# Kernel tuning notes

Hardware: AMD Instinct MI355X
Metric: run time of the kernel (lower is better)

## Reference

```python
import jax, jax.numpy as jnp
import numpy as np

D = 768
OUT = 196
EPS = 1e-6


def setup_inputs() -> dict:
    key = jax.random.key(0)
    k_x, k_w, k_b, k_g, k_beta = jax.random.split(key, 5)
    x = jax.random.normal(k_x, (16, 4096, D), dtype=jnp.float32)
    # LayerNorm affine params
    gamma = jnp.ones((D,), dtype=jnp.float32) + 0.01 * jax.random.normal(k_g, (D,), dtype=jnp.float32)
    beta = 0.01 * jax.random.normal(k_beta, (D,), dtype=jnp.float32)
    # Linear params (torch default init: U(-1/sqrt(D), 1/sqrt(D)))
    bound = 1.0 / np.sqrt(D)
    W = jax.random.uniform(k_w, (OUT, D), minval=-bound, maxval=bound, dtype=jnp.float32)
    b = jax.random.uniform(k_b, (OUT,), minval=-bound, maxval=bound, dtype=jnp.float32)
    return {"x": x, "gamma": gamma, "beta": beta, "W": W, "b": b}


def reference(x, gamma, beta, W, b):
    # LayerNorm over last dim (768), eps=1e-6, elementwise affine
    mean = jnp.mean(x, axis=-1, keepdims=True)
    var = jnp.mean(jnp.square(x - mean), axis=-1, keepdims=True)
    xn = (x - mean) * jax.lax.rsqrt(var + EPS) * gamma + beta
    # Linear 768 -> 196
    return jnp.einsum('bsd,od->bso', xn, W) + b
```

## Files before the change

### kernel.cpp

```cpp
#include <hip/hip_runtime.h>

#define DD   768
#define OUTN 196
#define MT   16
#define APAD 776
#define KT   24

typedef __attribute__((ext_vector_type(8))) _Float16 halfx8;
typedef __attribute__((ext_vector_type(4))) _Float16 halfx4;
typedef __attribute__((ext_vector_type(4))) float    f32x4;

__global__ __launch_bounds__(256) void wprep_kernel(const float* __restrict__ W,
                                                    _Float16* __restrict__ Wh) {
    int i = blockIdx.x * 256 + threadIdx.x;
    if (i < OUTN * DD) Wh[i] = (_Float16)W[i];
}

__global__ __launch_bounds__(256) void fused_ln_linear(
    const float* __restrict__ x, const float* __restrict__ gamma,
    const float* __restrict__ beta, const _Float16* __restrict__ Wh,
    const float* __restrict__ bias, float* __restrict__ out)
{
    __shared__ _Float16 Ahi[MT * APAD];
    __shared__ _Float16 Alo[MT * APAD];

    const int tid  = threadIdx.x;
    const int wv   = tid >> 6;
    const int lane = tid & 63;
    const long row0 = (long)blockIdx.x * MT;

    float4 g[3], be[3];
#pragma unroll
    for (int c = 0; c < 3; ++c) {
        const int d0 = c * 256 + lane * 4;
        g[c]  = *(const float4*)(gamma + d0);
        be[c] = *(const float4*)(beta  + d0);
    }

    {
        float4 xv[4][3];
#pragma unroll
        for (int t = 0; t < 4; ++t) {
            const float* xp = x + (row0 + wv * 4 + t) * DD;
#pragma unroll
            for (int c = 0; c < 3; ++c)
                xv[t][c] = *(const float4*)(xp + c * 256 + lane * 4);
        }
#pragma unroll
        for (int t = 0; t < 4; ++t) {
            float s = 0.f, ss = 0.f;
#pragma unroll
            for (int c = 0; c < 3; ++c) {
                const float4 v = xv[t][c];
                s  += v.x + v.y + v.z + v.w;
                ss += v.x * v.x + v.y * v.y + v.z * v.z + v.w * v.w;
            }
#pragma unroll
            for (int off = 32; off > 0; off >>= 1) {
                s  += __shfl_xor(s,  off);
                ss += __shfl_xor(ss, off);
            }
            const float mean = s * (1.f / DD);
            const float var  = ss * (1.f / DD) - mean * mean;
            const float rstd = rsqrtf(var + 1e-6f);
            const int r = wv * 4 + t;
#pragma unroll
            for (int c = 0; c < 3; ++c) {
                const float4 v = xv[t][c];
                float y0 = (v.x - mean) * rstd * g[c].x + be[c].x;
                float y1 = (v.y - mean) * rstd * g[c].y + be[c].y;
                float y2 = (v.z - mean) * rstd * g[c].z + be[c].z;
                float y3 = (v.w - mean) * rstd * g[c].w + be[c].w;
                halfx4 hi, lo;
                hi[0] = (_Float16)y0; lo[0] = (_Float16)(y0 - (float)hi[0]);
                hi[1] = (_Float16)y1; lo[1] = (_Float16)(y1 - (float)hi[1]);
                hi[2] = (_Float16)y2; lo[2] = (_Float16)(y2 - (float)hi[2]);
                hi[3] = (_Float16)y3; lo[3] = (_Float16)(y3 - (float)hi[3]);
                const int k0 = c * 256 + lane * 4;
                *(halfx4*)(&Ahi[r * APAD + k0]) = hi;
                *(halfx4*)(&Alo[r * APAD + k0]) = lo;
            }
        }
    }
    __syncthreads();

    const int cnt  = (wv == 0) ? 4 : 3;
    const int nt0  = (wv == 0) ? 0 : (1 + 3 * wv);
    const int ln16 = lane & 15;
    const int q    = lane >> 4;

    f32x4 acc[4];
#pragma unroll
    for (int i = 0; i < 4; ++i) acc[i] = (f32x4){0.f, 0.f, 0.f, 0.f};

    int ncol[4], nload[4];
    float bs[4];
#pragma unroll
    for (int i = 0; i < 4; ++i) {
        const int n = (nt0 + i) * 16 + ln16;
        ncol[i]  = n;
        nload[i] = n < OUTN ? n : OUTN - 1;
        bs[i]    = (n < OUTN) ? bias[n] : 0.f;
    }

    const _Float16* Aph = &Ahi[ln16 * APAD + q * 8];
    const _Float16* Apl = &Alo[ln16 * APAD + q * 8];
#pragma unroll
    for (int kt = 0; kt < KT; ++kt) {
        const halfx8 ah = *(const halfx8*)(Aph + kt * 32);
        const halfx8 al = *(const halfx8*)(Apl + kt * 32);
#pragma unroll
        for (int i = 0; i < 4; ++i) {
            if (i < cnt) {
                const halfx8 bf = *(const halfx8*)(Wh + nload[i] * DD + kt * 32 + q * 8);
                acc[i] = __builtin_amdgcn_mfma_f32_16x16x32_f16(ah, bf, acc[i], 0, 0, 0);
                acc[i] = __builtin_amdgcn_mfma_f32_16x16x32_f16(al, bf, acc[i], 0, 0, 0);
            }
        }
    }

    const long rbase = row0 + q * 4;
#pragma unroll
    for (int i = 0; i < 4; ++i) {
        if (i < cnt && ncol[i] < OUTN) {
#pragma unroll
            for (int rg = 0; rg < 4; ++rg)
                out[(rbase + rg) * OUTN + ncol[i]] = acc[i][rg] + bs[i];
        }
    }
}

extern "C" void kernel_launch(void* const* d_in, const int* in_sizes, int n_in,
                              void* d_out, int out_size, void* d_ws, size_t ws_size,
                              hipStream_t stream) {
    const float* x     = (const float*)d_in[0];
    const float* gamma = (const float*)d_in[1];
    const float* beta  = (const float*)d_in[2];
    const float* W     = (const float*)d_in[3];
    const float* b     = (const float*)d_in[4];
    float* out = (float*)d_out;
    _Float16* Wh = (_Float16*)d_ws;

    wprep_kernel<<<(OUTN * DD + 255) / 256, 256, 0, stream>>>(W, Wh);

    const long rows = 16L * 4096;
    fused_ln_linear<<<rows / MT, 256, 0, stream>>>(x, gamma, beta, Wh, b, out);
}
```

Baseline: 433.7 us.

## Pipeline LayerNorm staging with GEMM over K chunks using double-buffered LDS

The fused kernel now makes two passes over x. The first pass computes the row statistics. The second pass normalizes one 256-wide K chunk at a time into double-buffered shared memory, and the MFMA work on the previous chunk overlaps the next chunk's normalization. This shrinks LDS per block and register pressure (launch bounds now request 4 blocks), so occupancy should rise, but x is read from global memory twice and relies on cache hits. The weight conversion kernel is also vectorized to float4.

After: 416.1 us. 4.1% less time.

```diff
diff --git a/kernel.cpp b/kernel.cpp
--- a/kernel.cpp
+++ b/kernel.cpp
@@ -1,97 +1,73 @@
 #include <hip/hip_runtime.h>
 
-#define DD   768
-#define OUTN 196
-#define MT   16
-#define APAD 776
-#define KT   24
+#define DD    768
+#define OUTN  196
+#define MT    16
+#define KC    256
+#define APAD  264
+#define KTS   8
 
 typedef __attribute__((ext_vector_type(8))) _Float16 halfx8;
 typedef __attribute__((ext_vector_type(4))) _Float16 halfx4;
 typedef __attribute__((ext_vector_type(4))) float    f32x4;
 
-__global__ __launch_bounds__(256) void wprep_kernel(const float* __restrict__ W,
-                                                    _Float16* __restrict__ Wh) {
+__global__ __launch_bounds__(256) void wprep_kernel(const float4* __restrict__ W4,
+                                                    halfx4* __restrict__ Wh4) {
     int i = blockIdx.x * 256 + threadIdx.x;
-    if (i < OUTN * DD) Wh[i] = (_Float16)W[i];
+    if (i < OUTN * DD / 4) {
+        float4 v = W4[i];
+        halfx4 h;
+        h[0] = (_Float16)v.x; h[1] = (_Float16)v.y;
+        h[2] = (_Float16)v.z; h[3] = (_Float16)v.w;
+        Wh4[i] = h;
+    }
 }
 
-__global__ __launch_bounds__(256) void fused_ln_linear(
+__global__ __launch_bounds__(256, 4) void fused_ln_linear(
     const float* __restrict__ x, const float* __restrict__ gamma,
     const float* __restrict__ beta, const _Float16* __restrict__ Wh,
     const float* __restrict__ bias, float* __restrict__ out)
 {
-    __shared__ _Float16 Ahi[MT * APAD];
-    __shared__ _Float16 Alo[MT * APAD];
+    __shared__ _Float16 Ahi[2][MT * APAD];
+    __shared__ _Float16 Alo[2][MT * APAD];
 
     const int tid  = threadIdx.x;
     const int wv   = tid >> 6;
     const int lane = tid & 63;
     const long row0 = (long)blockIdx.x * MT;
+    const float* xrow = x + (row0 + wv * 4) * DD + lane * 4;
 
-    float4 g[3], be[3];
+    float mean[4], rstd[4];
+    {
+        float s[4], ss[4];
 #pragma unroll
-    for (int c = 0; c < 3; ++c) {
-        const int d0 = c * 256 + lane * 4;
-        g[c]  = *(const float4*)(gamma + d0);
-        be[c] = *(const float4*)(beta  + d0);
-    }
-
-    {
-        float4 xv[4][3];
+        for (int t = 0; t < 4; ++t) { s[t] = 0.f; ss[t] = 0.f; }
 #pragma unroll
         for (int t = 0; t < 4; ++t) {
-            const float* xp = x + (row0 + wv * 4 + t) * DD;
 #pragma unroll
-            for (int c = 0; c < 3; ++c)
-                xv[t][c] = *(const float4*)(xp + c * 256 + lane * 4);
+            for (int c = 0; c < 3; ++c) {
+                const float4 v = *(const float4*)(xrow + t * DD + c * KC);
+                s[t]  += v.x + v.y + v.z + v.w;
+                ss[t] += v.x * v.x + v.y * v.y + v.z * v.z + v.w * v.w;
+            }
         }
 #pragma unroll
         for (int t = 0; t < 4; ++t) {
-            float s = 0.f, ss = 0.f;
-#pragma unroll
-            for (int c = 0; c < 3; ++c) {
-                const float4 v = xv[t][c];
-                s  += v.x + v.y + v.z + v.w;
-                ss += v.x * v.x + v.y * v.y + v.z * v.z + v.w * v.w;
-            }
 #pragma unroll
             for (int off = 32; off > 0; off >>= 1) {
-                s  += __shfl_xor(s,  off);
-                ss += __shfl_xor(ss, off);
+                s[t]  += __shfl_xor(s[t],  off);
+                ss[t] += __shfl_xor(ss[t], off);
             }
-            const float mean = s * (1.f / DD);
-            const float var  = ss * (1.f / DD) - mean * mean;
-            const float rstd = rsqrtf(var + 1e-6f);
-            const int r = wv * 4 + t;
-#pragma unroll
-            for (int c = 0; c < 3; ++c) {
-                const float4 v = xv[t][c];
-                float y0 = (v.x - mean) * rstd * g[c].x + be[c].x;
-                float y1 = (v.y - mean) * rstd * g[c].y + be[c].y;
-                float y2 = (v.z - mean) * rstd * g[c].z + be[c].z;
-                float y3 = (v.w - mean) * rstd * g[c].w + be[c].w;
-                halfx4 hi, lo;
-                hi[0] = (_Float16)y0; lo[0] = (_Float16)(y0 - (float)hi[0]);
-                hi[1] = (_Float16)y1; lo[1] = (_Float16)(y1 - (float)hi[1]);
-                hi[2] = (_Float16)y2; lo[2] = (_Float16)(y2 - (float)hi[2]);
-                hi[3] = (_Float16)y3; lo[3] = (_Float16)(y3 - (float)hi[3]);
-                const int k0 = c * 256 + lane * 4;
-                *(halfx4*)(&Ahi[r * APAD + k0]) = hi;
-                *(halfx4*)(&Alo[r * APAD + k0]) = lo;
-            }
+            mean[t] = s[t] * (1.f / DD);
+            const float var = ss[t] * (1.f / DD) - mean[t] * mean[t];
+            rstd[t] = rsqrtf(var + 1e-6f);
         }
     }
-    __syncthreads();
 
     const int cnt  = (wv == 0) ? 4 : 3;
     const int nt0  = (wv == 0) ? 0 : (1 + 3 * wv);
     const int ln16 = lane & 15;
     const int q    = lane >> 4;
-
-    f32x4 acc[4];
-#pragma unroll
-    for (int i = 0; i < 4; ++i) acc[i] = (f32x4){0.f, 0.f, 0.f, 0.f};
 
     int ncol[4], nload[4];
     float bs[4];
@@ -99,25 +75,67 @@
     for (int i = 0; i < 4; ++i) {
         const int n = (nt0 + i) * 16 + ln16;
         ncol[i]  = n;
-        nload[i] = n < OUTN ? n : OUTN - 1;
+        nload[i] = (n < OUTN ? n : OUTN - 1) * DD;
         bs[i]    = (n < OUTN) ? bias[n] : 0.f;
     }
 
-    const _Float16* Aph = &Ahi[ln16 * APAD + q * 8];
-    const _Float16* Apl = &Alo[ln16 * APAD + q * 8];
+    f32x4 acc[4];
 #pragma unroll
-    for (int kt = 0; kt < KT; ++kt) {
-        const halfx8 ah = *(const halfx8*)(Aph + kt * 32);
-        const halfx8 al = *(const halfx8*)(Apl + kt * 32);
+    for (int i = 0; i < 4; ++i) acc[i] = (f32x4){0.f, 0.f, 0.f, 0.f};
+
+    auto stage_write = [&](int st, int buf) {
+        const int k0 = st * KC + lane * 4;
+        const float4 gv = *(const float4*)(gamma + k0);
+        const float4 bv = *(const float4*)(beta + k0);
 #pragma unroll
-        for (int i = 0; i < 4; ++i) {
-            if (i < cnt) {
-                const halfx8 bf = *(const halfx8*)(Wh + nload[i] * DD + kt * 32 + q * 8);
-                acc[i] = __builtin_amdgcn_mfma_f32_16x16x32_f16(ah, bf, acc[i], 0, 0, 0);
-                acc[i] = __builtin_amdgcn_mfma_f32_16x16x32_f16(al, bf, acc[i], 0, 0, 0);
+        for (int t = 0; t < 4; ++t) {
+            const float4 v = *(const float4*)(xrow + t * DD + st * KC);
+            const float y0 = (v.x - mean[t]) * rstd[t] * gv.x + bv.x;
+            const float y1 = (v.y - mean[t]) * rstd[t] * gv.y + bv.y;
+            const float y2 = (v.z - mean[t]) * rstd[t] * gv.z + bv.z;
+            const float y3 = (v.w - mean[t]) * rstd[t] * gv.w + bv.w;
+            halfx4 hi, lo;
+            hi[0] = (_Float16)y0; lo[0] = (_Float16)(y0 - (float)hi[0]);
+            hi[1] = (_Float16)y1; lo[1] = (_Float16)(y1 - (float)hi[1]);
+            hi[2] = (_Float16)y2; lo[2] = (_Float16)(y2 - (float)hi[2]);
+            hi[3] = (_Float16)y3; lo[3] = (_Float16)(y3 - (float)hi[3]);
+            const int r = wv * 4 + t;
+            *(halfx4*)(&Ahi[buf][r * APAD + lane * 4]) = hi;
+            *(halfx4*)(&Alo[buf][r * APAD + lane * 4]) = lo;
+        }
+    };
+
+    auto gemm_stage = [&](int st, int buf) {
+        const _Float16* Aph = &Ahi[buf][ln16 * APAD + q * 8];
+        const _Float16* Apl = &Alo[buf][ln16 * APAD + q * 8];
+#pragma unroll
+        for (int kt = 0; kt < KTS; ++kt) {
+            const halfx8 ah = *(const halfx8*)(Aph + kt * 32);
+            const halfx8 al = *(const halfx8*)(Apl + kt * 32);
+#pragma unroll
+            for (int i = 0; i < 4; ++i) {
+                if (i < cnt) {
+                    const halfx8 bf =
+                        *(const halfx8*)(Wh + nload[i] + st * KC + kt * 32 + q * 8);
+                    acc[i] = __builtin_amdgcn_mfma_f32_16x16x32_f16(ah, bf, acc[i], 0, 0, 0);
+                    acc[i] = __builtin_amdgcn_mfma_f32_16x16x32_f16(al, bf, acc[i], 0, 0, 0);
+                }
             }
         }
-    }
+    };
+
+    stage_write(0, 0);
+    __syncthreads();
+
+    stage_write(1, 1);
+    gemm_stage(0, 0);
+    __syncthreads();
+
+    stage_write(2, 0);
+    gemm_stage(1, 1);
+    __syncthreads();
+
+    gemm_stage(2, 0);
 
     const long rbase = row0 + q * 4;
 #pragma unroll
@@ -141,7 +159,8 @@
     float* out = (float*)d_out;
     _Float16* Wh = (_Float16*)d_ws;
 
-    wprep_kernel<<<(OUTN * DD + 255) / 256, 256, 0, stream>>>(W, Wh);
+    wprep_kernel<<<(OUTN * DD / 4 + 255) / 256, 256, 0, stream>>>(
+        (const float4*)W, (halfx4*)Wh);
 
     const long rows = 16L * 4096;
     fused_ln_linear<<<rows / MT, 256, 0, stream>>>(x, gamma, beta, Wh, b, out);
```
